# Kernel optimization log

Measured on AMD Instinct MI355X. Metric: run time of the kernel, lower is better.

## Reference

```python
import jax, jax.numpy as jnp
import numpy as np

# Config (from init_kwargs 'knn')
QUEUE_SIZE = 65536   # K
FEAT_DIM = 256       # D
BATCH = 512          # N (eval_sampling = 1.0 -> all samples used)
NUM_KNNS = 200
NUM_CLASSES = 1000
TEMPERATURE = 0.07


def _l2norm(x):
    return x / jnp.sqrt(jnp.sum(x * x, axis=-1, keepdims=True) + 1e-12)


def setup_inputs() -> dict:
    key = jax.random.key(0)
    k1, k2, k3, k4 = jax.random.split(key, 4)
    features = _l2norm(jax.random.normal(k1, (BATCH, FEAT_DIM), jnp.float32))
    labels = jax.random.randint(k2, (BATCH,), 0, NUM_CLASSES, jnp.int32)
    queue_features = _l2norm(jax.random.normal(k3, (QUEUE_SIZE, FEAT_DIM), jnp.float32))
    queue_labels = jax.random.randint(k4, (QUEUE_SIZE,), 0, NUM_CLASSES, jnp.int32)
    return {
        "features": features,
        "labels": labels,
        "queue_features": queue_features,
        "queue_labels": queue_labels,
        "queue_ptr": 0,
    }


def reference(features, labels, queue_features, queue_labels, queue_ptr):
    # ---- kNN accuracy (train branch, eval_sampling=1.0) ----
    sim = jnp.einsum('nc,kc->nk', features, queue_features)           # [N, K]
    sim_w, sim_idx = jax.lax.top_k(sim, k=NUM_KNNS)                   # [N, Kn]
    sim_w = jnp.exp(sim_w / TEMPERATURE)
    sim_labels = queue_labels[sim_idx]                                # [N, Kn] (vmapped gather)
    # weighted one-hot vote, expressed as a scatter-add (same math,
    # avoids the [N, Kn, C] one-hot intermediate)
    n = features.shape[0]
    pred_scores = jnp.zeros((n, NUM_CLASSES), sim_w.dtype)
    pred_scores = pred_scores.at[jnp.arange(n)[:, None], sim_labels].add(sim_w)
    pred_labels = jnp.argmax(pred_scores, axis=-1)
    accuracy = jnp.mean((pred_labels == labels).astype(jnp.float32))

    # ---- queue update (single device: all_gather == identity) ----
    batch_size = features.shape[0]
    inds = (jnp.arange(batch_size) + queue_ptr) % QUEUE_SIZE  # original asserts divisibility
    new_queue_features = queue_features.at[inds].set(features)
    new_queue_labels = queue_labels.at[inds].set(labels)
    new_queue_ptr = (queue_ptr + batch_size) % QUEUE_SIZE

    return accuracy, new_queue_features, new_queue_labels, new_queue_ptr
```

## Files before the change

kernel.cpp:

```cpp
#include <hip/hip_runtime.h>
#include <math.h>

#define NQ     65536
#define DIM    256
#define NBATCH 512
#define KNN    200
#define NCLS   1000
#define TSELF  0.155f
#define TSELH  0.150f
#define EPSF   0.0041f

#define GM  128
#define GK  32
#define NTN (NQ / GM)
#define KSTEPS (DIM / GK)

#define SUB   8
#define SCAP  256
#define CPAD  32

typedef unsigned short u16;
typedef unsigned long long u64;
typedef __attribute__((ext_vector_type(8))) short short8;
typedef __attribute__((ext_vector_type(4))) float f32x4;


__device__ __forceinline__ u16 f2bf(float x) {
  unsigned u = __float_as_uint(x);
  return (u16)((u + 0x7FFFu + ((u >> 16) & 1u)) >> 16);
}
__device__ __forceinline__ void load_lds16(const void* g, void* l) {
  __builtin_amdgcn_global_load_lds(
      (const __attribute__((address_space(1))) unsigned int*)g,
      (__attribute__((address_space(3))) unsigned int*)l, 16, 0, 0);
}
__device__ __forceinline__ void store_f4u(float* p, float4 v) {
  p[0] = v.x;
  *(float2*)(p + 1) = make_float2(v.y, v.z);
  p[3] = v.w;
}

__global__ __launch_bounds__(256) void prep_copy_kernel(
    const float* __restrict__ feat, const int* __restrict__ labels,
    const float* __restrict__ qf, const int* __restrict__ ql,
    const int* __restrict__ qptr,
    u16* __restrict__ Bb, u16* __restrict__ Ab,
    int* __restrict__ gcnt, float* __restrict__ out)
{
  const int idx = blockIdx.x * 256 + threadIdx.x;
  const int ptr = qptr[0];
  const long long NFEAT = (long long)NQ * DIM;

  {
    float4 qv = ((const float4*)qf)[idx];
    int row = idx >> 6;
    int c4  = idx & 63;
    int d = (row - ptr) & (NQ - 1);
    float4 ov = qv;
    if (d < NBATCH) ov = ((const float4*)feat)[d * 64 + c4];
    store_f4u(out + 1 + 4 * (long long)idx, ov);

    ushort4 h;
    h.x = f2bf(qv.x); h.y = f2bf(qv.y); h.z = f2bf(qv.z); h.w = f2bf(qv.w);
    ((ushort4*)Bb)[idx] = h;
  }

  if (idx < NBATCH * DIM / 4) {
    float4 v = ((const float4*)feat)[idx];
    ushort4 h;
    h.x = f2bf(v.x); h.y = f2bf(v.y); h.z = f2bf(v.z); h.w = f2bf(v.w);
    ((ushort4*)Ab)[idx] = h;
  }

  if (idx < NQ) {
    int d = (idx - ptr) & (NQ - 1);
    int v = (d < NBATCH) ? labels[d] : ql[idx];
    out[1 + NFEAT + idx] = (float)v;
  }

  if (idx < NBATCH * SUB) gcnt[idx * CPAD] = 0;
  if (idx == 0) {
    out[0] = 0.0f;
    out[1 + NFEAT + NQ] = (float)((ptr + NBATCH) & (NQ - 1));
  }
}

__global__ __launch_bounds__(256) void gemm_mfma(
    const u16* __restrict__ A, const u16* __restrict__ B,
    uint2* __restrict__ cand, int* __restrict__ gcnt)
{
  __shared__ u16 sA[2][GM][GK];
  __shared__ u16 sB[2][GM][GK];

  const int tid  = threadIdx.x;
  const int wave = tid >> 6, lane = tid & 63;
  const int d  = blockIdx.x;
  const int bm = (d >> 3) & 3;
  const int bn = (d & 7) | ((d >> 5) << 3);
  const int sub = d & 7;

  const u16* srcBase = ((wave < 2) ? (A + (size_t)bm * GM * DIM)
                                   : (B + (size_t)bn * GM * DIM))
                       + (size_t)(wave & 1) * 64 * DIM;
  const int kx = ((lane & 3) ^ ((lane >> 3) & 3)) * 8;
  const u16* src = srcBase + (lane >> 2) * DIM + kx;
  u16* dst0 = ((wave < 2) ? &sA[0][0][0] : &sB[0][0][0]) + (wave & 1) * 64 * GK;
  u16* dst1 = ((wave < 2) ? &sA[1][0][0] : &sB[1][0][0]) + (wave & 1) * 64 * GK;

  const int wm = (wave & 1) * 64, wn = (wave >> 1) * 64;
  const int fr = lane & 15;
  const int fq = lane >> 4;
  const int fqx = fq ^ ((fr >> 1) & 3);

  f32x4 acc[4][4] = {};

  {
    const u16* s = src;
#pragma unroll
    for (int g = 0; g < 4; ++g)
      load_lds16(s + g * 16 * DIM, dst0 + g * 512);
  }
  __syncthreads();

  for (int t = 0; t < KSTEPS; ++t) {
    const int cur = t & 1;
    if (t + 1 < KSTEPS) {
      const u16* s = src + (t + 1) * GK;
      u16* dl = cur ? dst0 : dst1;
#pragma unroll
      for (int g = 0; g < 4; ++g)
        load_lds16(s + g * 16 * DIM, dl + g * 512);
    }

    short8 a[4], b[4];
#pragma unroll
    for (int i = 0; i < 4; ++i) {
      a[i] = *(const short8*)&sA[cur][wm + i * 16 + fr][fqx * 8];
      b[i] = *(const short8*)&sB[cur][wn + i * 16 + fr][fqx * 8];
    }
#pragma unroll
    for (int i = 0; i < 4; ++i)
#pragma unroll
      for (int j = 0; j < 4; ++j)
        acc[i][j] = __builtin_amdgcn_mfma_f32_16x16x32_bf16(a[i], b[j], acc[i][j], 0, 0, 0);

    __syncthreads();
  }

  const int lrow0 = bm * GM + wm + fq * 4;
  const int ccol  = bn * GM + wn + fr;
#pragma unroll
  for (int i = 0; i < 4; ++i)
#pragma unroll
    for (int j = 0; j < 4; ++j)
#pragma unroll
      for (int r = 0; r < 4; ++r) {
        float v = acc[i][j][r];
        if (v > TSELF) {
          int grow = lrow0 + i * 16 + r;
          int col  = ccol + j * 16;
          int p = atomicAdd(&gcnt[(grow * SUB + sub) * CPAD], 1);
          if (p < SCAP)
            cand[((size_t)grow * SUB + sub) * SCAP + p] =
                make_uint2(__float_as_uint(v), (unsigned)col);
        }
      }
}

#define NBSEL 2048
#define CCAP  2048
#define LCAP  1024
#define NT    512
#define NG    (NT / 8)
#define NWV   (NT / 64)
#define BINW  ((1.001f - TSELH) / (float)NBSEL)

__global__ __launch_bounds__(NT, 4) void select_kernel(
    const uint2* __restrict__ cand, const int* __restrict__ gcnt,
    const int* __restrict__ labels,
    const int* __restrict__ qlab, const float* __restrict__ qf,
    const float* __restrict__ feat, float* __restrict__ out,
    float inv_n)
{
  __shared__ int   hist[NBSEL];
  __shared__ int   seg[NT];
  __shared__ int   wtot[NWV];
  __shared__ int   scnt[SUB];
  __shared__ float candV[CCAP];
  __shared__ int   candI[CCAP];
  __shared__ float votes[NCLS];
  __shared__ u64   ek[LCAP];
  __shared__ int   lst[LCAP];
  __shared__ float frow[DIM];
  __shared__ int   s_b, s_cnt, s_mb;
  __shared__ float s_chk;
  __shared__ u64   s_best;

  const int tid = threadIdx.x;
  const int row = blockIdx.x;

  bool fb = false;

  if (tid < DIM) frow[tid] = feat[(size_t)row * DIM + tid];
  for (int i = tid; i < NBSEL; i += NT) hist[i] = 0;
  for (int c = tid; c < NCLS; c += NT) votes[c] = 0.0f;
  if (tid < SUB) scnt[tid] = gcnt[(row * SUB + tid) * CPAD];
  if (tid == 0) { s_b = 0; s_mb = 0; s_best = 0ull; s_chk = -1.0f; s_cnt = 0; }
  __syncthreads();

  int n = 0;
  {
    bool ovf = false;
#pragma unroll
    for (int s = 0; s < SUB; ++s) {
      int c = scnt[s];
      if (c > SCAP) ovf = true;
      n += c < SCAP ? c : SCAP;
    }
    if (ovf || n < KNN) fb = true;
  }

  if (!fb) {
    {
      const int wv = tid >> 6, ln = tid & 63;
      int off = 0;
#pragma unroll
      for (int s = 0; s < SUB; ++s) {
        int c = scnt[s] < SCAP ? scnt[s] : SCAP;
        if (s < wv) off += c;
      }
      int c = scnt[wv] < SCAP ? scnt[wv] : SCAP;
      const uint2* rowc = cand + ((size_t)row * SUB + wv) * SCAP;
      for (int i = ln; i < c; i += 64) {
        uint2 e = rowc[i];
        candV[off + i] = __uint_as_float(e.x);
        candI[off + i] = (int)e.y;
      }
    }
    __syncthreads();

    const float SSCALE = 1.0f / BINW;
    for (int i = tid; i < n; i += NT) {
      int b = (int)((candV[i] - TSELH) * SSCALE);
      b = b < 0 ? 0 : (b > NBSEL - 1 ? NBSEL - 1 : b);
      atomicAdd(&hist[b], 1);
    }
    __syncthreads();
    {
      int s = 0;
#pragma unroll
      for (int i = 0; i < NBSEL / NT; ++i) s += hist[tid * (NBSEL / NT) + i];
      const int ln = tid & 63, wv = tid >> 6;
      int acc = s;
#pragma unroll
      for (int off = 1; off < 64; off <<= 1) {
        int o = __shfl_down(acc, off, 64);
        if (ln + off < 64) acc += o;
      }
      if (ln == 0) wtot[wv] = acc;
      __syncthreads();
      int addv = 0;
      for (int w = wv + 1; w < NWV; ++w) addv += wtot[w];
      seg[tid] = acc + addv;
    }
    __syncthreads();
    { int run = (tid < NT - 1) ? seg[tid + 1] : 0;
      for (int i = tid * (NBSEL / NT) + NBSEL / NT - 1;
           i >= tid * (NBSEL / NT); --i) {
        run += hist[i];
        if (run >= KNN) { atomicMax(&s_b, i); break; }
      } }
    __syncthreads();
    const int bstarA = s_b;
    const float thresh = TSELH + (float)bstarA * BINW - 2.0f * EPSF;

    for (int i = tid; i < n; i += NT) {
      if (candV[i] >= thresh) {
        int p = atomicAdd(&s_mb, 1);
        if (p < LCAP) lst[p] = i;
      }
    }
    __syncthreads();
    const int nr = s_mb;
    if (nr > LCAP || nr < KNN) fb = true;
    else {
      const int sub = tid & 7;
      const int grp = tid >> 3;
      const float4* fr4 = (const float4*)frow;

      float4 b0[8];
      if (grp < nr) {
        const float4* qr = (const float4*)(qf + (size_t)candI[lst[grp]] * DIM);
#pragma unroll
        for (int it = 0; it < 8; ++it) b0[it] = qr[sub + it * 8];
      }
      for (int k = grp; k < nr; k += NG) {
        const int kn = k + NG;
        float4 b1[8];
        if (kn < nr) {
          const float4* qr = (const float4*)(qf + (size_t)candI[lst[kn]] * DIM);
#pragma unroll
          for (int it = 0; it < 8; ++it) b1[it] = qr[sub + it * 8];
        }
        float p = 0.0f;
#pragma unroll
        for (int it = 0; it < 8; ++it) {
          float4 a = fr4[sub + it * 8];
          p = fmaf(a.x, b0[it].x, p); p = fmaf(a.y, b0[it].y, p);
          p = fmaf(a.z, b0[it].z, p); p = fmaf(a.w, b0[it].w, p);
        }
        p += __shfl_xor(p, 1, 64);
        p += __shfl_xor(p, 2, 64);
        p += __shfl_xor(p, 4, 64);
        if (sub == 0) candV[lst[k]] = p;
#pragma unroll
        for (int it = 0; it < 8; ++it) b0[it] = b1[it];
      }
      __syncthreads();

      for (int e = tid; e < nr; e += NT) {
        int ci = lst[e];
        ek[e] = ((u64)__float_as_uint(candV[ci]) << 32) |
                (u64)(0xFFFFFFFFu - (unsigned)candI[ci]);
      }
      __syncthreads();

      for (int e = tid; e < nr; e += NT) {
        u64 ke = ek[e];
        int rank = 0;
        for (int j = 0; j < nr; ++j) rank += (ek[j] > ke);
        if (rank < KNN) {
          float v = __uint_as_float((unsigned)(ke >> 32));
          int col = (int)(0xFFFFFFFFu - (unsigned)(ke & 0xFFFFFFFFull));
          atomicAdd(&votes[qlab[col]], expf(v * (1.0f / 0.07f)));
          if (rank == KNN - 1) s_chk = v;
        }
      }
      __syncthreads();
      if (s_chk < TSELF + EPSF) fb = true;
    }
  }

  if (fb) {
    for (int i = tid; i < NBSEL; i += NT) hist[i] = 0;
    if (tid == 0) { s_b = 0; s_cnt = 0; }
    __syncthreads();

    for (int q = tid; q < NQ; q += NT) {
      const float4* qr = (const float4*)(qf + (size_t)q * DIM);
      const float4* fr = (const float4*)frow;
      float s = 0.0f;
#pragma unroll
      for (int t = 0; t < DIM / 4; ++t) {
        float4 a = fr[t], b = qr[t];
        s = fmaf(a.x, b.x, s); s = fmaf(a.y, b.y, s);
        s = fmaf(a.z, b.z, s); s = fmaf(a.w, b.w, s);
      }
      int bin = (int)((s + 1.0f) * (NBSEL * 0.5f));
      bin = bin < 0 ? 0 : (bin > NBSEL - 1 ? NBSEL - 1 : bin);
      atomicAdd(&hist[bin], 1);
    }
    __syncthreads();

    { int s = 0;
#pragma unroll
      for (int i = 0; i < NBSEL / NT; ++i) s += hist[tid * (NBSEL / NT) + i];
      seg[tid] = s; }
    __syncthreads();
    for (int off = 1; off < NT; off <<= 1) {
      int t = (tid + off < NT) ? seg[tid + off] : 0;
      __syncthreads();
      seg[tid] += t;
      __syncthreads();
    }
    { int run = (tid < NT - 1) ? seg[tid + 1] : 0;
      for (int i = tid * (NBSEL / NT) + NBSEL / NT - 1;
           i >= tid * (NBSEL / NT); --i) {
        run += hist[i];
        if (run >= KNN) { atomicMax(&s_b, i); break; }
      } }
    __syncthreads();
    const int bstar = s_b;

    for (int q = tid; q < NQ; q += NT) {
      const float4* qr = (const float4*)(qf + (size_t)q * DIM);
      const float4* fr = (const float4*)frow;
      float s = 0.0f;
#pragma unroll
      for (int t = 0; t < DIM / 4; ++t) {
        float4 a = fr[t], b = qr[t];
        s = fmaf(a.x, b.x, s); s = fmaf(a.y, b.y, s);
        s = fmaf(a.z, b.z, s); s = fmaf(a.w, b.w, s);
      }
      int bin = (int)((s + 1.0f) * (NBSEL * 0.5f));
      bin = bin < 0 ? 0 : (bin > NBSEL - 1 ? NBSEL - 1 : bin);
      if (bin >= bstar) {
        int p = atomicAdd(&s_cnt, 1);
        if (p < CCAP) { candV[p] = s; candI[p] = q; }
      }
    }
    __syncthreads();
    int m = s_cnt < CCAP ? s_cnt : CCAP;

    int P = 256; while (P < m) P <<= 1;
    for (int i = tid; i < P; i += NT)
      if (i >= m) { candV[i] = -INFINITY; candI[i] = 0x7fffffff; }
    __syncthreads();
    for (int k = 2; k <= P; k <<= 1) {
      for (int j = k >> 1; j > 0; j >>= 1) {
        for (int i = tid; i < P; i += NT) {
          int ixj = i ^ j;
          if (ixj > i) {
            float va = candV[i], vb = candV[ixj];
            int ia = candI[i], ib = candI[ixj];
            bool aFirst = (va > vb) || (va == vb && ia < ib);
            bool up = ((i & k) == 0);
            if (up ? !aFirst : aFirst) {
              candV[i] = vb; candV[ixj] = va;
              candI[i] = ib; candI[ixj] = ia;
            }
          }
        }
        __syncthreads();
      }
    }

    for (int c = tid; c < NCLS; c += NT) votes[c] = 0.0f;
    __syncthreads();
    for (int i = tid; i < KNN; i += NT)
      atomicAdd(&votes[qlab[candI[i]]], expf(candV[i] * (1.0f / 0.07f)));
    __syncthreads();
  }

  u64 key = 0ull;
  for (int c = tid; c < NCLS; c += NT) {
    u64 k2 = ((u64)__float_as_uint(votes[c]) << 32) |
             (u64)(0xFFFFFFFFu - (unsigned)c);
    if (k2 > key) key = k2;
  }
  for (int off = 32; off > 0; off >>= 1) {
    u64 o = __shfl_down(key, off, 64);
    if (o > key) key = o;
  }
  if ((tid & 63) == 0) atomicMax(&s_best, key);
  __syncthreads();
  if (tid == 0) {
    int cls = (int)(0xFFFFFFFFu - (unsigned)(s_best & 0xFFFFFFFFull));
    if (cls == labels[row]) atomicAdd(out, inv_n);
  }
}

extern "C" void kernel_launch(void* const* d_in, const int* in_sizes, int n_in,
                              void* d_out, int out_size, void* d_ws, size_t ws_size,
                              hipStream_t stream)
{
  const float* features = (const float*)d_in[0];
  const int*   labels   = (const int*)d_in[1];
  const float* qfeat    = (const float*)d_in[2];
  const int*   qlab     = (const int*)d_in[3];
  const int*   qptr     = (const int*)d_in[4];
  float* out = (float*)d_out;

  int nbatch = in_sizes[0] / DIM;
  float inv_n = 1.0f / (float)nbatch;

  size_t bBytes = (size_t)NQ * DIM * 2;
  u16*   Bb   = (u16*)d_ws;
  uint2* cand = (uint2*)((char*)d_ws + bBytes);
  int*   gcnt = (int*)((char*)cand + (size_t)NBATCH * SUB * SCAP * 8);
  u16*   Ab   = (u16*)(gcnt + (size_t)NBATCH * SUB * CPAD);

  prep_copy_kernel<<<NQ * DIM / 4 / 256, 256, 0, stream>>>(
      features, labels, qfeat, qlab, qptr, Bb, Ab, gcnt, out);

  gemm_mfma<<<(NBATCH / GM) * (NQ / GM), 256, 0, stream>>>(
      Ab, Bb, cand, gcnt);

  select_kernel<<<nbatch, NT, 0, stream>>>(cand, gcnt, labels, qlab,
                                           qfeat, features, out, inv_n);
}
```

Baseline: 203.4 us.

## Triple-buffer GEMM LDS staging with prefetch depth two and manual waitcnt barriers

Changes the bf16 MFMA similarity GEMM from double to triple buffering in LDS, issuing global-to-LDS loads two K-steps ahead. Each iteration now uses a single barrier with an explicit partial vmcnt wait instead of two __syncthreads, and the K loop is fully unrolled. The aim is to hide global load latency behind more MFMA work. In exchange, LDS use grows by half, which may lower occupancy, and correctness now depends on the hand-written waitcnt counts matching the number of outstanding loads.

```diff
diff --git a/kernel.cpp b/kernel.cpp
--- a/kernel.cpp
+++ b/kernel.cpp
@@ -89,8 +89,8 @@
     const u16* __restrict__ A, const u16* __restrict__ B,
     uint2* __restrict__ cand, int* __restrict__ gcnt)
 {
-  __shared__ u16 sA[2][GM][GK];
-  __shared__ u16 sB[2][GM][GK];
+  __shared__ u16 sA[3][GM][GK];
+  __shared__ u16 sB[3][GM][GK];
 
   const int tid  = threadIdx.x;
   const int wave = tid >> 6, lane = tid & 63;
@@ -104,8 +104,6 @@
                        + (size_t)(wave & 1) * 64 * DIM;
   const int kx = ((lane & 3) ^ ((lane >> 3) & 3)) * 8;
   const u16* src = srcBase + (lane >> 2) * DIM + kx;
-  u16* dst0 = ((wave < 2) ? &sA[0][0][0] : &sB[0][0][0]) + (wave & 1) * 64 * GK;
-  u16* dst1 = ((wave < 2) ? &sA[1][0][0] : &sB[1][0][0]) + (wave & 1) * 64 * GK;
 
   const int wm = (wave & 1) * 64, wn = (wave >> 1) * 64;
   const int fr = lane & 15;
@@ -114,23 +112,30 @@
 
   f32x4 acc[4][4] = {};
 
-  {
-    const u16* s = src;
-#pragma unroll
-    for (int g = 0; g < 4; ++g)
-      load_lds16(s + g * 16 * DIM, dst0 + g * 512);
-  }
-  __syncthreads();
-
+#define STAGE(q, t)                                                          \
+  {                                                                          \
+    const u16* s_ = src + (t) * GK;                                          \
+    u16* dl_ = ((wave < 2) ? &sA[(q)][0][0] : &sB[(q)][0][0]) +              \
+               (wave & 1) * 64 * GK;                                         \
+    _Pragma("unroll")                                                        \
+    for (int g = 0; g < 4; ++g)                                              \
+      load_lds16(s_ + g * 16 * DIM, dl_ + g * 512);                          \
+  }
+
+  STAGE(0, 0)
+  STAGE(1, 1)
+
+#pragma unroll
   for (int t = 0; t < KSTEPS; ++t) {
-    const int cur = t & 1;
-    if (t + 1 < KSTEPS) {
-      const u16* s = src + (t + 1) * GK;
-      u16* dl = cur ? dst0 : dst1;
-#pragma unroll
-      for (int g = 0; g < 4; ++g)
-        load_lds16(s + g * 16 * DIM, dl + g * 512);
-    }
+    const int cur = t % 3;
+    __builtin_amdgcn_sched_barrier(0);
+    if (t < KSTEPS - 1)
+      asm volatile("s_waitcnt vmcnt(4) lgkmcnt(0)\n\ts_barrier" ::: "memory");
+    else
+      asm volatile("s_waitcnt vmcnt(0) lgkmcnt(0)\n\ts_barrier" ::: "memory");
+    __builtin_amdgcn_sched_barrier(0);
+
+    if (t + 2 < KSTEPS) STAGE((t + 2) % 3, t + 2)
 
     short8 a[4], b[4];
 #pragma unroll
@@ -143,9 +148,8 @@
 #pragma unroll
       for (int j = 0; j < 4; ++j)
         acc[i][j] = __builtin_amdgcn_mfma_f32_16x16x32_bf16(a[i], b[j], acc[i][j], 0, 0, 0);
-
-    __syncthreads();
-  }
+  }
+#undef STAGE
 
   const int lrow0 = bm * GM + wm + fq * 4;
   const int ccol  = bn * GM + wn + fr;
```

After: 213.9 us. +5.2%, slower.

## Move queue-feature output copy from prep kernel into extra select-kernel blocks

Applied to the files above, without the earlier changes.

The 64 MB float copy of the updated queue features into the output is removed from the prep kernel. It is now done by extra blocks appended to the select kernel's grid, so the bandwidth-heavy copy can overlap with the latency-bound per-row top-k selection instead of sitting in front of the GEMM. The copy blocks reuse the select kernel's large shared-memory footprint, which may limit how many run concurrently, and they re-read qf a second time.

```diff
diff --git a/kernel.cpp b/kernel.cpp
--- a/kernel.cpp
+++ b/kernel.cpp
@@ -18,6 +18,8 @@
 #define SUB   8
 #define SCAP  256
 #define CPAD  32
+
+#define NCOPY 512
 
 typedef unsigned short u16;
 typedef unsigned long long u64;
@@ -53,13 +55,6 @@
 
   {
     float4 qv = ((const float4*)qf)[idx];
-    int row = idx >> 6;
-    int c4  = idx & 63;
-    int d = (row - ptr) & (NQ - 1);
-    float4 ov = qv;
-    if (d < NBATCH) ov = ((const float4*)feat)[d * 64 + c4];
-    store_f4u(out + 1 + 4 * (long long)idx, ov);
-
     ushort4 h;
     h.x = f2bf(qv.x); h.y = f2bf(qv.y); h.z = f2bf(qv.z); h.w = f2bf(qv.w);
     ((ushort4*)Bb)[idx] = h;
@@ -179,8 +174,8 @@
     const uint2* __restrict__ cand, const int* __restrict__ gcnt,
     const int* __restrict__ labels,
     const int* __restrict__ qlab, const float* __restrict__ qf,
-    const float* __restrict__ feat, float* __restrict__ out,
-    float inv_n)
+    const float* __restrict__ feat, const int* __restrict__ qptr,
+    float* __restrict__ out, float inv_n, int nbatch)
 {
   __shared__ int   hist[NBSEL];
   __shared__ int   seg[NT];
@@ -198,6 +193,22 @@
 
   const int tid = threadIdx.x;
   const int row = blockIdx.x;
+
+  if (row >= nbatch) {
+    const int cb = row - nbatch;
+    const int ptr = qptr[0];
+    const long long base = (long long)cb * (NQ / NCOPY) * (DIM / 4);
+    for (int t = tid; t < (NQ / NCOPY) * (DIM / 4); t += NT) {
+      long long idx = base + t;
+      int r  = (int)(idx >> 6);
+      int c4 = (int)(idx & 63);
+      int dd = (r - ptr) & (NQ - 1);
+      float4 v = (dd < NBATCH) ? ((const float4*)feat)[dd * 64 + c4]
+                               : ((const float4*)qf)[idx];
+      store_f4u(out + 1 + 4 * idx, v);
+    }
+    return;
+  }
 
   bool fb = false;
 
@@ -476,6 +487,6 @@
   gemm_mfma<<<(NBATCH / GM) * (NQ / GM), 256, 0, stream>>>(
       Ab, Bb, cand, gcnt);
 
-  select_kernel<<<nbatch, NT, 0, stream>>>(cand, gcnt, labels, qlab,
-                                           qfeat, features, out, inv_n);
-}
+  select_kernel<<<nbatch + NCOPY, NT, 0, stream>>>(
+      cand, gcnt, labels, qlab, qfeat, features, qptr, out, inv_n, nbatch);
+}
```

After: 212.5 us. 1.04x slower.
